# Performance work log

Hardware: AMD Instinct MI355X
Metric: run time of the kernel (lower is better)

## Reference

```python
import jax, jax.numpy as jnp
import numpy as np

D_MODEL = 1024
NUM_HEADS = 16
D_K = D_MODEL // NUM_HEADS
THETA = 10000.0
BATCH = 4
SEQ = 2048


def _apply_rope(t, positions, theta):
    # t: (B, H, S, d_k); positions: (S,) int
    d_k = t.shape[-1]
    inv_freq = theta ** (-jnp.arange(0, d_k, 2, dtype=jnp.float32) / d_k)  # (d_k/2,)
    angles = positions.astype(jnp.float32)[:, None] * inv_freq[None, :]    # (S, d_k/2)
    cos = jnp.cos(angles)
    sin = jnp.sin(angles)
    x1 = t[..., 0::2]
    x2 = t[..., 1::2]
    r1 = x1 * cos - x2 * sin
    r2 = x1 * sin + x2 * cos
    # interleave back to (..., d_k)
    return jnp.stack([r1, r2], axis=-1).reshape(t.shape)


def setup_inputs() -> dict:
    key = jax.random.key(0)
    k0, k1, k2, k3, k4 = jax.random.split(key, 5)
    scale = 1.0 / np.sqrt(D_MODEL)
    return {
        "x": jax.random.normal(k0, (BATCH, SEQ, D_MODEL), dtype=jnp.float32),
        "wq": jax.random.normal(k1, (D_MODEL, D_MODEL), dtype=jnp.float32) * scale,
        "wk": jax.random.normal(k2, (D_MODEL, D_MODEL), dtype=jnp.float32) * scale,
        "wv": jax.random.normal(k3, (D_MODEL, D_MODEL), dtype=jnp.float32) * scale,
        "wo": jax.random.normal(k4, (D_MODEL, D_MODEL), dtype=jnp.float32) * scale,
        "token_positions": jnp.arange(SEQ, dtype=jnp.int32),
    }


def reference(x, wq, wk, wv, wo, token_positions):
    B, S, _ = x.shape
    H, dk = NUM_HEADS, D_K

    def proj(w):
        # Linear: y = x @ w.T, then split heads -> (B, H, S, d_k)
        y = jnp.einsum("bsd,ed->bse", x, w)
        return y.reshape(B, S, H, dk).transpose(0, 2, 1, 3)

    q = proj(wq)
    k = proj(wk)
    v = proj(wv)

    q = _apply_rope(q, token_positions, THETA)
    k = _apply_rope(k, token_positions, THETA)

    scores = jnp.einsum("bhqd,bhkd->bhqk", q, k) / jnp.sqrt(jnp.float32(dk))
    causal = jnp.tril(jnp.ones((S, S), dtype=bool))  # (S, S)
    scores = jnp.where(causal[None, None, :, :], scores, -jnp.inf)
    attn = jax.nn.softmax(scores, axis=-1)
    out = jnp.einsum("bhqk,bhkd->bhqd", attn, v)        # (B, H, S, d_k)
    out = out.transpose(0, 2, 1, 3).reshape(B, S, H * dk)
    return jnp.einsum("bse,de->bsd", out, wo)
```

## Files before the change

kernel.cpp:

```cpp
#include <hip/hip_runtime.h>
#include <hip/hip_bf16.h>

#define D_MODEL 1024
#define NHEADS 16
#define DKH 64
#define BATCH 4
#define SEQ 2048
#define BH_ (BATCH*NHEADS)
#define MROWS (BATCH*SEQ)

typedef __attribute__((ext_vector_type(8))) short bf16x8;
typedef __attribute__((ext_vector_type(4))) float f32x4;
typedef __attribute__((ext_vector_type(4))) short short4v;

static __device__ __forceinline__ unsigned short f2b(float f){
  union { float f; unsigned u; } v; v.f = f;
  unsigned u = v.u;
  return (unsigned short)((u + 0x7FFFu + ((u >> 16) & 1u)) >> 16);
}
static __device__ __forceinline__ float b2f(unsigned short h){
  union { unsigned u; float f; } v; v.u = ((unsigned)h) << 16; return v.f;
}

static __device__ __forceinline__ f32x4 mfma16(bf16x8 a, bf16x8 b, f32x4 c){
  return __builtin_amdgcn_mfma_f32_16x16x32_bf16(a, b, c, 0, 0, 0);
}

static __device__ __forceinline__ float fexp2(float x){
#if __has_builtin(__builtin_amdgcn_exp2f)
  return __builtin_amdgcn_exp2f(x);
#else
  float r; asm("v_exp_f32 %0, %1" : "=v"(r) : "v"(x)); return r;
#endif
}

static __device__ __forceinline__ void gload_lds16(const unsigned short* g, void* l){
  __builtin_amdgcn_global_load_lds((const __attribute__((address_space(1))) void*)g,
                                   (__attribute__((address_space(3))) void*)l,
                                   16, 0, 0);
}

__global__ void cvt_bf16_kernel(const float* __restrict__ src,
                                unsigned short* __restrict__ dst, int n4){
  int i = blockIdx.x*blockDim.x + threadIdx.x;
  if (i >= n4) return;
  float4 f = ((const float4*)src)[i];
  short4v o;
  o.x = (short)f2b(f.x); o.y = (short)f2b(f.y);
  o.z = (short)f2b(f.z); o.w = (short)f2b(f.w);
  ((short4v*)dst)[i] = o;
}

__global__ void cvt_w_kernel(const float* __restrict__ wq, const float* __restrict__ wk,
                             const float* __restrict__ wv, const float* __restrict__ wo,
                             unsigned short* __restrict__ wcat, unsigned short* __restrict__ wob){
  int i = blockIdx.x*blockDim.x + threadIdx.x;
  int seg = i >> 18;
  int j = i & 0x3FFFF;
  const float* s = (seg==0) ? wq : (seg==1) ? wk : (seg==2) ? wv : wo;
  unsigned short* d = (seg < 3) ? (wcat + ((size_t)seg << 20)) : wob;
  float4 f = ((const float4*)s)[j];
  short4v o;
  o.x = (short)f2b(f.x); o.y = (short)f2b(f.y);
  o.z = (short)f2b(f.z); o.w = (short)f2b(f.w);
  ((short4v*)d)[j] = o;
}

__global__ void rope_tab_kernel(const int* __restrict__ pos, float2* __restrict__ tab){
  int i = blockIdx.x*blockDim.x + threadIdx.x;
  if (i >= SEQ*32) return;
  int s = i >> 5, j = i & 31;
  float p = (float)pos[s];
  float fr = expf(-((float)(2*j) * (1.0f/DKH)) * 9.210340371976184f);
  float sn, cs;
  sincosf(p * fr, &sn, &cs);
  tab[i] = make_float2(cs, sn);
}

#define BM 128
#define BN 128
#define BKG 64

template<int MODE>
__global__ __launch_bounds__(256, 3) void gemm_nt(const unsigned short* __restrict__ A,
                                                  const unsigned short* __restrict__ Bw,
                                                  void* __restrict__ C,
                                                  const float2* __restrict__ tab,
                                                  int M, int N, int K)
{
  __shared__ unsigned short smem[BM*BKG + BN*BKG];
  unsigned short* As = smem;
  unsigned short* Bs = smem + BM*BKG;
  const int t = threadIdx.x;
  const int lane = t & 63;
  const int wv = t >> 6;
  const int wr = wv >> 1, wc = wv & 1;
  const int l15 = lane & 15, l4 = lane >> 4;
  const int m0 = blockIdx.y*BM, n0 = blockIdx.x*BN;

  f32x4 acc[4][4] = {};

  const int srow = lane >> 3;
  const int sce  = (lane & 7) * 8;

  for (int kt = 0; kt < K; kt += BKG){
    __syncthreads();
    #pragma unroll
    for (int jj = 0; jj < 4; ++jj){
      const int i = wv + jj*4;
      const int row = i*8 + srow;
      gload_lds16(A  + (size_t)(m0 + row)*K + kt + sce, (char*)As + i*1024 + lane*16);
      gload_lds16(Bw + (size_t)(n0 + row)*K + kt + sce, (char*)Bs + i*1024 + lane*16);
    }
    __syncthreads();
    #pragma unroll
    for (int kk = 0; kk < 2; ++kk){
      bf16x8 af[4], bfr[4];
      #pragma unroll
      for (int mi = 0; mi < 4; ++mi)
        af[mi] = *(const bf16x8*)((const char*)As + (wr*64 + mi*16 + l15)*128 + kk*64 + l4*16);
      #pragma unroll
      for (int ni = 0; ni < 4; ++ni)
        bfr[ni] = *(const bf16x8*)((const char*)Bs + (wc*64 + ni*16 + l15)*128 + kk*64 + l4*16);
      #pragma unroll
      for (int mi = 0; mi < 4; ++mi)
        #pragma unroll
        for (int ni = 0; ni < 4; ++ni)
          acc[mi][ni] = mfma16(af[mi], bfr[ni], acc[mi][ni]);
    }
  }

  if (MODE == 1){
    #pragma unroll
    for (int mi = 0; mi < 4; ++mi)
      #pragma unroll
      for (int ni = 0; ni < 4; ++ni)
        #pragma unroll
        for (int r = 0; r < 4; ++r){
          int row = m0 + wr*64 + mi*16 + l4*4 + r;
          int col = n0 + wc*64 + ni*16 + l15;
          ((float*)C)[(size_t)row*N + col] = acc[mi][ni][r];
        }
    return;
  }

  const int which = n0 >> 10;

  if (which == 2){
    __syncthreads();
    #pragma unroll
    for (int mi = 0; mi < 4; ++mi)
      #pragma unroll
      for (int ni = 0; ni < 4; ++ni){
        int d_l = wc*64 + ni*16 + l15;
        int s0  = wr*64 + mi*16 + l4*4;
        short4v pk;
        pk.x = (short)f2b(acc[mi][ni][0]);
        pk.y = (short)f2b(acc[mi][ni][1]);
        pk.z = (short)f2b(acc[mi][ni][2]);
        pk.w = (short)f2b(acc[mi][ni][3]);
        int byte = d_l*256 + ((s0*2) ^ ((d_l & 7) << 4));
        *(short4v*)((char*)smem + byte) = pk;
      }
    __syncthreads();
    const int d_l = t >> 1;
    const int half = t & 1;
    const int hb = (n0 & 1023) >> 6;
    const int b = m0 >> 11;
    const int s_b = m0 & (SEQ-1);
    const int bh = b*NHEADS + hb + (d_l >> 6);
    const int d = d_l & 63;
    unsigned short* vt = (unsigned short*)C + 2*((size_t)BH_*SEQ*DKH);
    unsigned short* dst = vt + ((size_t)bh*DKH + d)*SEQ + s_b + half*64;
    #pragma unroll
    for (int c = 0; c < 8; ++c){
      int sl = half*64 + c*8;
      int byte = d_l*256 + ((sl*2) ^ ((d_l & 7) << 4));
      *(bf16x8*)(dst + c*8) = *(const bf16x8*)((const char*)smem + byte);
    }
    return;
  }

  unsigned short* qk = (unsigned short*)C + (size_t)which*((size_t)BH_*SEQ*DKH);
  #pragma unroll
  for (int ni = 0; ni < 4; ++ni){
    int col = n0 + wc*64 + ni*16 + l15;
    int cl = col & 1023;
    int h = cl >> 6, dd = cl & (DKH-1);
    int j = dd >> 1;
    bool odd = dd & 1;
    #pragma unroll
    for (int mi = 0; mi < 4; ++mi)
      #pragma unroll
      for (int r = 0; r < 4; ++r){
        int row = m0 + wr*64 + mi*16 + l4*4 + r;
        int b = row >> 11, s = row & (SEQ-1);
        float2 cst = tab[s*32 + j];
        float xv = acc[mi][ni][r];
        float pv = __shfl_xor(xv, 1);
        float res = odd ? fmaf(xv, cst.x,  pv*cst.y)
                        : fmaf(xv, cst.x, -pv*cst.y);
        qk[((size_t)(b*NHEADS + h)*SEQ + s)*DKH + dd] = f2b(res);
      }
  }
}

#define QW 32
#define QB 128
#define KVB 64

__global__ __launch_bounds__(256, 3) void attn_kernel(const unsigned short* __restrict__ Q,
                                                      const unsigned short* __restrict__ Kw,
                                                      const unsigned short* __restrict__ Vt,
                                                      unsigned short* __restrict__ Ob)
{
  __shared__ unsigned short Ks[2][KVB*64];
  __shared__ unsigned short Vs[2][KVB*64];
  __shared__ unsigned short Ps[4][QW*KVB];

  const int t = threadIdx.x;
  const int lane = t & 63;
  const int wv = t >> 6;
  const int l15 = lane & 15, l4 = lane >> 4;

  const int bid = blockIdx.x;
  const int bh = bid & (BH_-1);
  const int qt = (SEQ/QB - 1) - (bid >> 6);
  const int q0 = qt * QB;
  const int qw0 = q0 + wv*QW;

  const unsigned short* kg = Kw + (size_t)bh*SEQ*DKH;
  const unsigned short* vg = Vt + (size_t)bh*DKH*SEQ;
  const unsigned short* qg = Q  + ((size_t)bh*SEQ + qw0)*DKH;

  bf16x8 qa[2][2];
  #pragma unroll
  for (int qi = 0; qi < 2; ++qi)
    #pragma unroll
    for (int c = 0; c < 2; ++c)
      qa[qi][c] = *(const bf16x8*)(qg + (qi*16 + l15)*DKH + c*32 + l4*8);

  const float KAPPA = 0.125f * 1.4426950408889634f;
  float m_r[2] = {-1e30f, -1e30f};
  float l_r[2] = {0.f, 0.f};
  f32x4 oacc[2][4] = {};

  const int srow = t >> 3;
  const int scb  = (t & 7) * 16;
  const int sko  = scb ^ ((srow & 7) << 4);
  const size_t vstride = (size_t)SEQ * 2;

  const int ntB   = q0/KVB + 2;
  const int twmax = (qw0 + QW - 1) >> 6;

  bf16x8 kl0, kl1, vl0, vl1;
  {
    const char* ksrc = (const char*)kg;
    const char* vsrc = (const char*)vg;
    kl0 = *(const bf16x8*)(ksrc + srow*128 + sko);
    kl1 = *(const bf16x8*)(ksrc + (srow+32)*128 + sko);
    vl0 = *(const bf16x8*)(vsrc + (size_t)srow*vstride + sko);
    vl1 = *(const bf16x8*)(vsrc + (size_t)(srow+32)*vstride + sko);
    *(bf16x8*)((char*)Ks[0] + srow*128 + scb)      = kl0;
    *(bf16x8*)((char*)Ks[0] + (srow+32)*128 + scb) = kl1;
    *(bf16x8*)((char*)Vs[0] + srow*128 + scb)      = vl0;
    *(bf16x8*)((char*)Vs[0] + (srow+32)*128 + scb) = vl1;
  }

  for (int tt = 0; tt < ntB; ++tt){
    const int cur = tt & 1;
    __syncthreads();
    const bool pre = (tt + 1 < ntB);
    if (pre){
      const size_t kvoff = (size_t)(tt+1) * KVB;
      const char* ksrc = (const char*)kg + kvoff*128;
      const char* vsrc = (const char*)vg + kvoff*2;
      kl0 = *(const bf16x8*)(ksrc + srow*128 + sko);
      kl1 = *(const bf16x8*)(ksrc + (srow+32)*128 + sko);
      vl0 = *(const bf16x8*)(vsrc + (size_t)srow*vstride + sko);
      vl1 = *(const bf16x8*)(vsrc + (size_t)(srow+32)*vstride + sko);
    }

    if (tt <= twmax){
      const char* kb = (const char*)Ks[cur];
      const char* vb = (const char*)Vs[cur];
      char* pb = (char*)Ps[wv];
      const int sw = (l15 & 7) << 4;
      const bool needmask = (tt == twmax);

      f32x4 sacc[4][2];
      #pragma unroll
      for (int kt = 0; kt < 4; ++kt){
        const int krow = kt*16 + l15;
        bf16x8 kf0 = *(const bf16x8*)(kb + krow*128 + ((l4*16) ^ sw));
        bf16x8 kf1 = *(const bf16x8*)(kb + krow*128 + ((64 + l4*16) ^ sw));
        #pragma unroll
        for (int qi = 0; qi < 2; ++qi){
          f32x4 a = {};
          a = mfma16(kf0, qa[qi][0], a);
          a = mfma16(kf1, qa[qi][1], a);
          sacc[kt][qi] = a;
        }
      }

      const int kv0 = tt * KVB;
      #pragma unroll
      for (int qi = 0; qi < 2; ++qi){
        const int qrow = qw0 + qi*16 + l15;
        float p[16];
        float mloc = -1e30f;
        #pragma unroll
        for (int kt = 0; kt < 4; ++kt)
          #pragma unroll
          for (int r = 0; r < 4; ++r){
            float x = sacc[kt][qi][r] * KAPPA;
            if (needmask){
              int kvg = kv0 + kt*16 + l4*4 + r;
              x = (kvg > qrow) ? -1e30f : x;
            }
            p[kt*4+r] = x;
            mloc = fmaxf(mloc, x);
          }
        mloc = fmaxf(mloc, __shfl_xor(mloc, 16));
        mloc = fmaxf(mloc, __shfl_xor(mloc, 32));

        const bool skip = __all(mloc - m_r[qi] <= 12.0f);
        float mn = m_r[qi];
        if (!skip){
          mn = fmaxf(m_r[qi], mloc);
          float alpha = fexp2(m_r[qi] - mn);
          m_r[qi] = mn;
          l_r[qi] *= alpha;
          float ar[4];
          #pragma unroll
          for (int r = 0; r < 4; ++r) ar[r] = __shfl(alpha, l4*4 + r);
          #pragma unroll
          for (int dt = 0; dt < 4; ++dt)
            #pragma unroll
            for (int r = 0; r < 4; ++r) oacc[qi][dt][r] *= ar[r];
        }
        float rs = 0.f;
        #pragma unroll
        for (int i = 0; i < 16; ++i){ p[i] = fexp2(p[i] - mn); rs += p[i]; }
        rs += __shfl_xor(rs, 16);
        rs += __shfl_xor(rs, 32);
        l_r[qi] += rs;

        char* pr = pb + (qi*16 + l15)*128;
        #pragma unroll
        for (int kt = 0; kt < 4; ++kt){
          unsigned u0, u1;
          asm("v_cvt_pk_bf16_f32 %0, %1, %2" : "=v"(u0) : "v"(p[kt*4+0]), "v"(p[kt*4+1]));
          asm("v_cvt_pk_bf16_f32 %0, %1, %2" : "=v"(u1) : "v"(p[kt*4+2]), "v"(p[kt*4+3]));
          unsigned long long uu = (unsigned long long)u0 | ((unsigned long long)u1 << 32);
          *(unsigned long long*)(pr + ((kt*32 + l4*8) ^ sw)) = uu;
        }
      }

      bf16x8 pa[2][2];
      #pragma unroll
      for (int qi = 0; qi < 2; ++qi){
        const char* pr = pb + (qi*16 + l15)*128;
        pa[qi][0] = *(const bf16x8*)(pr + ((l4*16) ^ sw));
        pa[qi][1] = *(const bf16x8*)(pr + ((64 + l4*16) ^ sw));
      }

      #pragma unroll
      for (int dt = 0; dt < 4; ++dt){
        const int vrow = dt*16 + l15;
        bf16x8 vf0 = *(const bf16x8*)(vb + vrow*128 + ((l4*16) ^ sw));
        bf16x8 vf1 = *(const bf16x8*)(vb + vrow*128 + ((64 + l4*16) ^ sw));
        #pragma unroll
        for (int qi = 0; qi < 2; ++qi){
          oacc[qi][dt] = mfma16(pa[qi][0], vf0, oacc[qi][dt]);
          oacc[qi][dt] = mfma16(pa[qi][1], vf1, oacc[qi][dt]);
        }
      }
    }

    if (pre){
      char* kd = (char*)Ks[cur^1];
      char* vd = (char*)Vs[cur^1];
      *(bf16x8*)(kd + srow*128 + scb)      = kl0;
      *(bf16x8*)(kd + (srow+32)*128 + scb) = kl1;
      *(bf16x8*)(vd + srow*128 + scb)      = vl0;
      *(bf16x8*)(vd + (srow+32)*128 + scb) = vl1;
    }
  }

  const int b = bh >> 4, h = bh & 15;
  #pragma unroll
  for (int qi = 0; qi < 2; ++qi){
    float inv = 1.0f / l_r[qi];
    float ir[4];
    #pragma unroll
    for (int r = 0; r < 4; ++r) ir[r] = __shfl(inv, l4*4 + r);
    #pragma unroll
    for (int r = 0; r < 4; ++r){
      int q = qw0 + qi*16 + l4*4 + r;
      unsigned short* orow = Ob + ((size_t)(b*SEQ + q))*D_MODEL + h*DKH;
      #pragma unroll
      for (int dt = 0; dt < 4; ++dt)
        orow[dt*16 + l15] = f2b(oacc[qi][dt][r] * ir[r]);
    }
  }
}

extern "C" void kernel_launch(void* const* d_in, const int* in_sizes, int n_in,
                              void* d_out, int out_size, void* d_ws, size_t ws_size,
                              hipStream_t stream)
{
  const float* x  = (const float*)d_in[0];
  const float* wq = (const float*)d_in[1];
  const float* wk = (const float*)d_in[2];
  const float* wv = (const float*)d_in[3];
  const float* wo = (const float*)d_in[4];
  const int* tp   = (const int*)d_in[5];
  float* out = (float*)d_out;

  unsigned short* ws = (unsigned short*)d_ws;
  size_t off = 0;
  unsigned short* xb   = ws + off; off += (size_t)MROWS*D_MODEL;
  unsigned short* wcat = ws + off; off += (size_t)3*D_MODEL*D_MODEL;
  unsigned short* wob  = ws + off; off += (size_t)D_MODEL*D_MODEL;
  unsigned short* qw   = ws + off; off += (size_t)BH_*SEQ*DKH;
  unsigned short* kw   = ws + off; off += (size_t)BH_*SEQ*DKH;
  unsigned short* vt   = ws + off; off += (size_t)BH_*SEQ*DKH;
  unsigned short* ao   = ws + off; off += (size_t)BH_*SEQ*DKH;
  float2* tab = (float2*)(ws + off); off += (size_t)SEQ*32*4;

  cvt_bf16_kernel<<<(MROWS*D_MODEL/4 + 255)/256, 256, 0, stream>>>(x, xb, MROWS*D_MODEL/4);
  cvt_w_kernel<<<(4*262144 + 255)/256, 256, 0, stream>>>(wq, wk, wv, wo, wcat, wob);
  rope_tab_kernel<<<(SEQ*32 + 255)/256, 256, 0, stream>>>(tp, tab);

  gemm_nt<0><<<dim3(3*D_MODEL/BN, MROWS/BM), 256, 0, stream>>>(xb, wcat, qw, tab,
                                                               MROWS, 3*D_MODEL, D_MODEL);

  attn_kernel<<<BH_*(SEQ/QB), 256, 0, stream>>>(qw, kw, vt, ao);

  gemm_nt<1><<<dim3(D_MODEL/BN, MROWS/BM), 256, 0, stream>>>(ao, wob, out, nullptr,
                                                             MROWS, D_MODEL, D_MODEL);
}
```

Measured before the change: 260.5 us.

## Fuse prep kernels, fold softmax scale into Q, add setprio and max3 reductions

Merges the three preprocessing launches (x conversion, weight conversion, RoPE table) into one kernel that dispatches on block index, removing two launches. Folds the 1/sqrt(dk)*log2(e) softmax scale into the Q projection epilogue so the attention loop skips a per-score multiply. Adds s_setprio around the MFMA blocks in attention and computes the row max with three-input max trees. Pre-scaling Q before bf16 rounding slightly changes numerics.

Result: no change. 263.5 us (+1.2%).

```diff
diff --git a/kernel.cpp b/kernel.cpp
--- a/kernel.cpp
+++ b/kernel.cpp
@@ -33,6 +33,9 @@
   float r; asm("v_exp_f32 %0, %1" : "=v"(r) : "v"(x)); return r;
 #endif
 }
+static __device__ __forceinline__ float max3f(float a, float b, float c){
+  return fmaxf(fmaxf(a, b), c);
+}
 
 static __device__ __forceinline__ void gload_lds16(const unsigned short* g, void* l){
   __builtin_amdgcn_global_load_lds((const __attribute__((address_space(1))) void*)g,
@@ -40,41 +43,44 @@
                                    16, 0, 0);
 }
 
-__global__ void cvt_bf16_kernel(const float* __restrict__ src,
-                                unsigned short* __restrict__ dst, int n4){
-  int i = blockIdx.x*blockDim.x + threadIdx.x;
-  if (i >= n4) return;
-  float4 f = ((const float4*)src)[i];
-  short4v o;
-  o.x = (short)f2b(f.x); o.y = (short)f2b(f.y);
-  o.z = (short)f2b(f.z); o.w = (short)f2b(f.w);
-  ((short4v*)dst)[i] = o;
-}
-
-__global__ void cvt_w_kernel(const float* __restrict__ wq, const float* __restrict__ wk,
-                             const float* __restrict__ wv, const float* __restrict__ wo,
-                             unsigned short* __restrict__ wcat, unsigned short* __restrict__ wob){
-  int i = blockIdx.x*blockDim.x + threadIdx.x;
-  int seg = i >> 18;
-  int j = i & 0x3FFFF;
-  const float* s = (seg==0) ? wq : (seg==1) ? wk : (seg==2) ? wv : wo;
-  unsigned short* d = (seg < 3) ? (wcat + ((size_t)seg << 20)) : wob;
-  float4 f = ((const float4*)s)[j];
-  short4v o;
-  o.x = (short)f2b(f.x); o.y = (short)f2b(f.y);
-  o.z = (short)f2b(f.z); o.w = (short)f2b(f.w);
-  ((short4v*)d)[j] = o;
-}
-
-__global__ void rope_tab_kernel(const int* __restrict__ pos, float2* __restrict__ tab){
-  int i = blockIdx.x*blockDim.x + threadIdx.x;
-  if (i >= SEQ*32) return;
-  int s = i >> 5, j = i & 31;
-  float p = (float)pos[s];
-  float fr = expf(-((float)(2*j) * (1.0f/DKH)) * 9.210340371976184f);
-  float sn, cs;
-  sincosf(p * fr, &sn, &cs);
-  tab[i] = make_float2(cs, sn);
+#define QSCALE 0.1803368801111137f
+
+__global__ void prep_kernel(const float* __restrict__ x,
+                            const float* __restrict__ wq, const float* __restrict__ wk,
+                            const float* __restrict__ wv, const float* __restrict__ wo,
+                            const int* __restrict__ pos,
+                            unsigned short* __restrict__ xb,
+                            unsigned short* __restrict__ wcat,
+                            unsigned short* __restrict__ wob,
+                            float2* __restrict__ tab){
+  const int bid = blockIdx.x;
+  if (bid < 8192){
+    int i = bid*256 + threadIdx.x;
+    float4 f = ((const float4*)x)[i];
+    short4v o;
+    o.x = (short)f2b(f.x); o.y = (short)f2b(f.y);
+    o.z = (short)f2b(f.z); o.w = (short)f2b(f.w);
+    ((short4v*)xb)[i] = o;
+  } else if (bid < 8192 + 4096){
+    int i = (bid - 8192)*256 + threadIdx.x;
+    int seg = i >> 18;
+    int j = i & 0x3FFFF;
+    const float* s = (seg==0) ? wq : (seg==1) ? wk : (seg==2) ? wv : wo;
+    unsigned short* d = (seg < 3) ? (wcat + ((size_t)seg << 20)) : wob;
+    float4 f = ((const float4*)s)[j];
+    short4v o;
+    o.x = (short)f2b(f.x); o.y = (short)f2b(f.y);
+    o.z = (short)f2b(f.z); o.w = (short)f2b(f.w);
+    ((short4v*)d)[j] = o;
+  } else {
+    int i = (bid - 12288)*256 + threadIdx.x;
+    int s = i >> 5, j = i & 31;
+    float p = (float)pos[s];
+    float fr = expf(-((float)(2*j) * (1.0f/DKH)) * 9.210340371976184f);
+    float sn, cs;
+    sincosf(p * fr, &sn, &cs);
+    tab[i] = make_float2(cs, sn);
+  }
 }
 
 #define BM 128
@@ -182,6 +188,7 @@
   }
 
   unsigned short* qk = (unsigned short*)C + (size_t)which*((size_t)BH_*SEQ*DKH);
+  const float oscale = (which == 0) ? QSCALE : 1.0f;
   #pragma unroll
   for (int ni = 0; ni < 4; ++ni){
     int col = n0 + wc*64 + ni*16 + l15;
@@ -200,7 +207,7 @@
         float pv = __shfl_xor(xv, 1);
         float res = odd ? fmaf(xv, cst.x,  pv*cst.y)
                         : fmaf(xv, cst.x, -pv*cst.y);
-        qk[((size_t)(b*NHEADS + h)*SEQ + s)*DKH + dd] = f2b(res);
+        qk[((size_t)(b*NHEADS + h)*SEQ + s)*DKH + dd] = f2b(res * oscale);
       }
   }
 }
@@ -240,7 +247,6 @@
     for (int c = 0; c < 2; ++c)
       qa[qi][c] = *(const bf16x8*)(qg + (qi*16 + l15)*DKH + c*32 + l4*8);
 
-  const float KAPPA = 0.125f * 1.4426950408889634f;
   float m_r[2] = {-1e30f, -1e30f};
   float l_r[2] = {0.f, 0.f};
   f32x4 oacc[2][4] = {};
@@ -289,6 +295,7 @@
       const bool needmask = (tt == twmax);
 
       f32x4 sacc[4][2];
+      __builtin_amdgcn_s_setprio(1);
       #pragma unroll
       for (int kt = 0; kt < 4; ++kt){
         const int krow = kt*16 + l15;
@@ -302,25 +309,30 @@
           sacc[kt][qi] = a;
         }
       }
+      __builtin_amdgcn_s_setprio(0);
 
       const int kv0 = tt * KVB;
       #pragma unroll
       for (int qi = 0; qi < 2; ++qi){
         const int qrow = qw0 + qi*16 + l15;
         float p[16];
-        float mloc = -1e30f;
         #pragma unroll
         for (int kt = 0; kt < 4; ++kt)
           #pragma unroll
           for (int r = 0; r < 4; ++r){
-            float x = sacc[kt][qi][r] * KAPPA;
+            float xx = sacc[kt][qi][r];
             if (needmask){
               int kvg = kv0 + kt*16 + l4*4 + r;
-              x = (kvg > qrow) ? -1e30f : x;
+              xx = (kvg > qrow) ? -1e30f : xx;
             }
-            p[kt*4+r] = x;
-            mloc = fmaxf(mloc, x);
+            p[kt*4+r] = xx;
           }
+        float t0 = max3f(p[0], p[1], p[2]);
+        float t1 = max3f(p[3], p[4], p[5]);
+        float t2 = max3f(p[6], p[7], p[8]);
+        float t3 = max3f(p[9], p[10], p[11]);
+        float t4 = max3f(p[12], p[13], p[14]);
+        float mloc = fmaxf(max3f(t0, t1, t2), max3f(t3, t4, p[15]));
         mloc = fmaxf(mloc, __shfl_xor(mloc, 16));
         mloc = fmaxf(mloc, __shfl_xor(mloc, 32));
 
@@ -365,6 +377,7 @@
         pa[qi][1] = *(const bf16x8*)(pr + ((64 + l4*16) ^ sw));
       }
 
+      __builtin_amdgcn_s_setprio(1);
       #pragma unroll
       for (int dt = 0; dt < 4; ++dt){
         const int vrow = dt*16 + l15;
@@ -376,6 +389,7 @@
           oacc[qi][dt] = mfma16(pa[qi][1], vf1, oacc[qi][dt]);
         }
       }
+      __builtin_amdgcn_s_setprio(0);
     }
 
     if (pre){
@@ -429,9 +443,7 @@
   unsigned short* ao   = ws + off; off += (size_t)BH_*SEQ*DKH;
   float2* tab = (float2*)(ws + off); off += (size_t)SEQ*32*4;
 
-  cvt_bf16_kernel<<<(MROWS*D_MODEL/4 + 255)/256, 256, 0, stream>>>(x, xb, MROWS*D_MODEL/4);
-  cvt_w_kernel<<<(4*262144 + 255)/256, 256, 0, stream>>>(wq, wk, wv, wo, wcat, wob);
-  rope_tab_kernel<<<(SEQ*32 + 255)/256, 256, 0, stream>>>(tp, tab);
+  prep_kernel<<<12544, 256, 0, stream>>>(x, wq, wk, wv, wo, tp, xb, wcat, wob, tab);
 
   gemm_nt<0><<<dim3(3*D_MODEL/BN, MROWS/BM), 256, 0, stream>>>(xb, wcat, qw, tab,
                                                                MROWS, 3*D_MODEL, D_MODEL);
```
